# Optimization experiments

Measured on AMD Instinct MI355X. Metric: run time of the kernel, lower is better.

The kernel has to match this reference:

```python
import jax, jax.numpy as jnp
import numpy as np

B, T, E, H = 1, 2048, 2048, 32
D = E // H  # head_dim = 64


def alibi_bias(n_heads, t_q, t_k, dtype):
    # slopes: 2^(-8*(h+1)/n_heads) for power-of-two head counts
    slopes = jnp.power(2.0, -8.0 * jnp.arange(1, n_heads + 1, dtype=jnp.float32) / n_heads)
    i = jnp.arange(t_q)[:, None] + (t_k - t_q)  # absolute query positions
    j = jnp.arange(t_k)[None, :]
    rel = (j - i).astype(dtype)                 # [t_q, t_k], <=0 on/below diagonal
    return (slopes[:, None, None] * rel).astype(dtype)  # [H, t_q, t_k]


def setup_inputs() -> dict:
    key = jax.random.key(0)
    kx, kq, kk, kv, ko = jax.random.split(key, 5)
    s = E ** -0.5
    x = jax.random.normal(kx, (B, T, E), dtype=jnp.float32)
    Wq = jax.random.normal(kq, (E, E), dtype=jnp.float32) * s
    Wk = jax.random.normal(kk, (D, E), dtype=jnp.float32) * s
    Wv = jax.random.normal(kv, (D, E), dtype=jnp.float32) * s
    Wo = jax.random.normal(ko, (E, E), dtype=jnp.float32) * s
    # causal mask: True where attention is disallowed (j > i)
    attention_mask = jnp.triu(jnp.ones((T, T), dtype=bool), k=1)[None, None]  # [1,1,T,T]
    return {"x": x, "Wq": Wq, "Wk": Wk, "Wv": Wv, "Wo": Wo, "attention_mask": attention_mask}


def reference(x, Wq, Wk, Wv, Wo, attention_mask):
    b, t, _ = x.shape
    scale = D ** -0.5
    q = (x @ Wq.T).reshape(b, t, H, D).transpose(0, 2, 1, 3)  # [b,H,t,D]
    k = x @ Wk.T                                              # [b,t,D] (single KV head)
    v = x @ Wv.T                                              # [b,t,D]
    attn = jnp.einsum('bhtd,bsd->bhts', q * scale, k)         # [b,H,t,t]
    attn = attn + alibi_bias(H, t, t, attn.dtype)[None]
    attn = jnp.where(attention_mask, jnp.asarray(-10000.0, attn.dtype), attn)
    w = jax.nn.softmax(attn, axis=-1)
    out = jnp.einsum('bhts,bsd->bhtd', w, v)                  # [b,H,t,D]
    out = out.transpose(0, 2, 1, 3).reshape(b, t, E)
    return out @ Wo.T
```

## Files before the change

### kernel.cpp

```cpp
#include <hip/hip_runtime.h>
#include <stdint.h>

typedef __bf16 bf16;
typedef __bf16 bf16x4 __attribute__((ext_vector_type(4)));
typedef __bf16 bf16x8 __attribute__((ext_vector_type(8)));
typedef short short4v __attribute__((ext_vector_type(4)));
typedef float floatx4 __attribute__((ext_vector_type(4)));

#define MFMA32(a, b, c) __builtin_amdgcn_mfma_f32_16x16x32_bf16((a), (b), (c), 0, 0, 0)

__device__ __forceinline__ floatx4 mfma16(bf16x4 a, bf16x4 b, floatx4 c) {
  return __builtin_amdgcn_mfma_f32_16x16x16bf16_1k(
      __builtin_bit_cast(short4v, a), __builtin_bit_cast(short4v, b), c, 0, 0, 0);
}

__device__ __forceinline__ void gload16(const void* g, void* l) {
  __builtin_amdgcn_global_load_lds(
      (const __attribute__((address_space(1))) void*)g,
      (__attribute__((address_space(3))) void*)l, 16, 0, 0);
}

__device__ __forceinline__ bf16x8 load8(const float* p) {
  float4 lo = *(const float4*)p;
  float4 hi = *(const float4*)(p + 4);
  bf16x8 r;
  r[0] = (bf16)lo.x; r[1] = (bf16)lo.y; r[2] = (bf16)lo.z; r[3] = (bf16)lo.w;
  r[4] = (bf16)hi.x; r[5] = (bf16)hi.y; r[6] = (bf16)hi.z; r[7] = (bf16)hi.w;
  return r;
}

__global__ __launch_bounds__(256) void conv3(const float* __restrict__ a, bf16* __restrict__ ab,
                                             const float* __restrict__ b, bf16* __restrict__ bb,
                                             const float* __restrict__ c, bf16* __restrict__ cb) {
  const int i = blockIdx.x * 256 + threadIdx.x;
  const float* src = blockIdx.y == 0 ? a : (blockIdx.y == 1 ? b : c);
  bf16* dst = blockIdx.y == 0 ? ab : (blockIdx.y == 1 ? bb : cb);
  ((bf16x8*)dst)[i] = load8(src + (size_t)i * 8);
}

__global__ __launch_bounds__(256) void pack_kv(const float* __restrict__ Kf,
                                               const float* __restrict__ Vf,
                                               bf16* __restrict__ Kb,
                                               bf16* __restrict__ Vtb) {
  int i = blockIdx.x * 256 + threadIdx.x;
  if (i < 2048 * 64) {
    Kb[i] = (bf16)Kf[i];
    const int t = i >> 6, d = i & 63;
    Vtb[(size_t)d * 2048 + t] = (bf16)Vf[i];
  }
}

template <typename TC>
__global__ __launch_bounds__(256) void gemm_bt_a(const bf16* __restrict__ A,
                                                 const bf16* __restrict__ B,
                                                 TC* __restrict__ C,
                                                 int M, int N, int K) {
  __shared__ __align__(16) bf16 As[2][128 * 32];
  __shared__ __align__(16) bf16 Bs[2][128 * 32];
  const int tid = threadIdx.x;
  const int wave = tid >> 6, lane = tid & 63;
  const int quad = lane >> 4, l16 = lane & 15;
  const int m0 = blockIdx.y * 128, n0 = blockIdx.x * 128;
  const int wm = (wave >> 1) * 64, wn = (wave & 1) * 64;

  floatx4 acc[4][4];
#pragma unroll
  for (int i = 0; i < 4; i++)
#pragma unroll
    for (int j = 0; j < 4; j++) acc[i][j] = (floatx4)0.f;

  const int srow = tid >> 2, scol = (tid & 3) * 8;
  const bf16* Ap = A + (size_t)(m0 + srow) * K + scol;
  const bf16* Bp = B + (size_t)(n0 + srow) * K + scol;

  auto stage = [&](int k0, int buf) {
    char* a = (char*)As[buf] + tid * 16;
    char* b = (char*)Bs[buf] + tid * 16;
    gload16(Ap + k0, a);
    gload16(Ap + (size_t)64 * K + k0, a + 4096);
    gload16(Bp + k0, b);
    gload16(Bp + (size_t)64 * K + k0, b + 4096);
  };
  auto compute = [&](int buf) {
    bf16x8 af[4], bfr[4];
#pragma unroll
    for (int mt = 0; mt < 4; mt++)
      af[mt] = *(const bf16x8*)(&As[buf][(wm + mt * 16 + l16) * 32 + quad * 8]);
#pragma unroll
    for (int nt = 0; nt < 4; nt++)
      bfr[nt] = *(const bf16x8*)(&Bs[buf][(wn + nt * 16 + l16) * 32 + quad * 8]);
#pragma unroll
    for (int mt = 0; mt < 4; mt++)
#pragma unroll
      for (int nt = 0; nt < 4; nt++)
        acc[mt][nt] = MFMA32(af[mt], bfr[nt], acc[mt][nt]);
  };

  stage(0, 0);
  for (int k0 = 0; k0 < K; k0 += 64) {
    __syncthreads();
    if (k0 + 32 < K) stage(k0 + 32, 1);
    compute(0);
    __syncthreads();
    if (k0 + 64 < K) stage(k0 + 64, 0);
    compute(1);
  }

#pragma unroll
  for (int mt = 0; mt < 4; mt++) {
#pragma unroll
    for (int nt = 0; nt < 4; nt++) {
      const int col = n0 + wn + nt * 16 + l16;
      const int row = m0 + wm + mt * 16 + quad * 4;
#pragma unroll
      for (int r = 0; r < 4; r++)
        C[(size_t)(row + r) * N + col] = (TC)acc[mt][nt][r];
    }
  }
}

__global__ __launch_bounds__(256) void kv_gemm(const bf16* __restrict__ xb,
                                               const float* __restrict__ Wk,
                                               const float* __restrict__ Wv,
                                               float* __restrict__ Kf,
                                               float* __restrict__ Vf) {
  __shared__ __align__(16) bf16 As[128 * 40];
  __shared__ __align__(16) bf16 Bs[128 * 40];
  const int tid = threadIdx.x;
  const int wave = tid >> 6, lane = tid & 63;
  const int quad = lane >> 4, l16 = lane & 15;
  const int m0 = blockIdx.y * 128;
  const int kbeg = blockIdx.x * 256, kend = kbeg + 256;
  const int wm = (wave >> 1) * 64, wn = (wave & 1) * 64;

  floatx4 acc[4][4];
#pragma unroll
  for (int i = 0; i < 4; i++)
#pragma unroll
    for (int j = 0; j < 4; j++) acc[i][j] = (floatx4)0.f;

  const int sr = tid >> 2, sc = (tid & 3) * 8;

  for (int k0 = kbeg; k0 < kend; k0 += 32) {
    __syncthreads();
#pragma unroll
    for (int rr = 0; rr < 2; rr++) {
      const int row = sr + rr * 64;
      *(bf16x8*)(&As[row * 40 + sc]) =
          *(const bf16x8*)(&xb[(size_t)(m0 + row) * 2048 + k0 + sc]);
      const float* bsrc = (row < 64) ? &Wk[(size_t)row * 2048 + k0 + sc]
                                     : &Wv[(size_t)(row - 64) * 2048 + k0 + sc];
      *(bf16x8*)(&Bs[row * 40 + sc]) = load8(bsrc);
    }
    __syncthreads();

    bf16x8 af[4], bfr[4];
#pragma unroll
    for (int mt = 0; mt < 4; mt++)
      af[mt] = *(const bf16x8*)(&As[(wm + mt * 16 + l16) * 40 + quad * 8]);
#pragma unroll
    for (int nt = 0; nt < 4; nt++)
      bfr[nt] = *(const bf16x8*)(&Bs[(wn + nt * 16 + l16) * 40 + quad * 8]);
#pragma unroll
    for (int mt = 0; mt < 4; mt++)
#pragma unroll
      for (int nt = 0; nt < 4; nt++)
        acc[mt][nt] = MFMA32(af[mt], bfr[nt], acc[mt][nt]);
  }

#pragma unroll
  for (int mt = 0; mt < 4; mt++) {
#pragma unroll
    for (int nt = 0; nt < 4; nt++) {
      const int col = wn + nt * 16 + l16;
      const int row = m0 + wm + mt * 16 + quad * 4;
      float* dst = (col < 64) ? &Kf[(size_t)row * 64 + col]
                              : &Vf[(size_t)row * 64 + (col - 64)];
#pragma unroll
      for (int r = 0; r < 4; r++) atomicAdd(dst + (size_t)r * 64, acc[mt][nt][r]);
    }
  }
}

__global__ __launch_bounds__(256) void attn_kernel(const bf16* __restrict__ Q,
                                                   const bf16* __restrict__ Kb,
                                                   const bf16* __restrict__ Vtb,
                                                   bf16* __restrict__ O) {
  __shared__ __align__(16) bf16 Ks[64 * 72];
  __shared__ __align__(16) bf16 Vt[64 * 72];
  const int tid = threadIdx.x;
  const int wq = tid >> 6, lane = tid & 63;
  const int quad = lane >> 4, l16 = lane & 15;
  const int h = blockIdx.y;
  const float scale2 = 0.125f * 1.44269504f;
  const float slope2 = exp2f(-0.25f * (float)(h + 1)) * 1.44269504f;

  float cst[4][4];
#pragma unroll
  for (int mt = 0; mt < 4; mt++)
#pragma unroll
    for (int r = 0; r < 4; r++)
      cst[mt][r] = slope2 * (float)(mt * 16 + quad * 4 + r);

  const int r0 = tid >> 3, c0 = (tid & 7) * 8;

  auto run_tile = [&](int t) {
    const int qi = t * 64 + wq * 16 + l16;
    bf16x8 qf[2];
#pragma unroll
    for (int kk = 0; kk < 2; kk++)
      qf[kk] = *(const bf16x8*)(&Q[(size_t)qi * 2048 + h * 64 + kk * 32 + quad * 8]);

    floatx4 oacc[4];
#pragma unroll
    for (int dt = 0; dt < 4; dt++) oacc[dt] = (floatx4)0.f;
    float l_part = 0.f;

    bf16x8 kreg[2], vreg[2];
    kreg[0] = *(const bf16x8*)(&Kb[(size_t)r0 * 64 + c0]);
    kreg[1] = *(const bf16x8*)(&Kb[(size_t)(r0 + 32) * 64 + c0]);
    vreg[0] = *(const bf16x8*)(&Vtb[(size_t)r0 * 2048 + c0]);
    vreg[1] = *(const bf16x8*)(&Vtb[(size_t)(r0 + 32) * 2048 + c0]);

    for (int kt = 0; kt <= t; kt++) {
      __syncthreads();
      *(bf16x8*)(&Ks[r0 * 72 + c0]) = kreg[0];
      *(bf16x8*)(&Ks[(r0 + 32) * 72 + c0]) = kreg[1];
      *(bf16x8*)(&Vt[r0 * 72 + c0]) = vreg[0];
      *(bf16x8*)(&Vt[(r0 + 32) * 72 + c0]) = vreg[1];
      __syncthreads();
      if (kt < t) {
        const int kn = (kt + 1) * 64;
        kreg[0] = *(const bf16x8*)(&Kb[(size_t)(kn + r0) * 64 + c0]);
        kreg[1] = *(const bf16x8*)(&Kb[(size_t)(kn + r0 + 32) * 64 + c0]);
        vreg[0] = *(const bf16x8*)(&Vtb[(size_t)r0 * 2048 + kn + c0]);
        vreg[1] = *(const bf16x8*)(&Vtb[(size_t)(r0 + 32) * 2048 + kn + c0]);
      }
      const int k0 = kt * 64;

      floatx4 s[4];
#pragma unroll
      for (int mt = 0; mt < 4; mt++) s[mt] = (floatx4)0.f;
#pragma unroll
      for (int kk = 0; kk < 2; kk++) {
#pragma unroll
        for (int mt = 0; mt < 4; mt++) {
          bf16x8 kf = *(const bf16x8*)(&Ks[(mt * 16 + l16) * 72 + kk * 32 + quad * 8]);
          s[mt] = MFMA32(kf, qf[kk], s[mt]);
        }
      }

      const float base = slope2 * (float)(k0 - qi);
      bf16x4 pb[4];
      if (kt < t) {
#pragma unroll
        for (int mt = 0; mt < 4; mt++) {
          bf16x4 tb;
#pragma unroll
          for (int r = 0; r < 4; r++) {
            const float p = exp2f(__builtin_fmaf(s[mt][r], scale2, base + cst[mt][r]));
            l_part += p;
            tb[r] = (bf16)p;
          }
          pb[mt] = tb;
        }
      } else {
        const int qloc = qi - k0;
#pragma unroll
        for (int mt = 0; mt < 4; mt++) {
          bf16x4 tb;
#pragma unroll
          for (int r = 0; r < 4; r++) {
            const int moff = mt * 16 + quad * 4 + r;
            float p = exp2f(__builtin_fmaf(s[mt][r], scale2, base + cst[mt][r]));
            p = (moff <= qloc) ? p : 0.f;
            l_part += p;
            tb[r] = (bf16)p;
          }
          pb[mt] = tb;
        }
      }

#pragma unroll
      for (int dt = 0; dt < 4; dt++)
#pragma unroll
        for (int mt = 0; mt < 4; mt++) {
          const bf16x4 va = *(const bf16x4*)(&Vt[(dt * 16 + l16) * 72 + mt * 16 + quad * 4]);
          oacc[dt] = mfma16(va, pb[mt], oacc[dt]);
        }
    }

    float lf = l_part;
    lf += __shfl_xor(lf, 16);
    lf += __shfl_xor(lf, 32);
    const float linv = 1.0f / lf;
#pragma unroll
    for (int dt = 0; dt < 4; dt++) {
      bf16x4 ob;
#pragma unroll
      for (int r = 0; r < 4; r++) ob[r] = (bf16)(oacc[dt][r] * linv);
      *(bf16x4*)(&O[(size_t)qi * 2048 + h * 64 + dt * 16 + quad * 4]) = ob;
    }
  };

  run_tile(blockIdx.x);
  run_tile(31 - blockIdx.x);
}

extern "C" void kernel_launch(void* const* d_in, const int* in_sizes, int n_in,
                              void* d_out, int out_size, void* d_ws,
                              size_t ws_size, hipStream_t stream) {
  (void)in_sizes; (void)n_in; (void)out_size; (void)ws_size;
  const float* x = (const float*)d_in[0];
  const float* Wq = (const float*)d_in[1];
  const float* Wk = (const float*)d_in[2];
  const float* Wv = (const float*)d_in[3];
  const float* Wo = (const float*)d_in[4];
  float* out = (float*)d_out;

  const size_t NE = (size_t)2048 * 2048;
  bf16* xb = (bf16*)d_ws;
  bf16* Wqb = xb + NE;
  bf16* Wob = Wqb + NE;
  bf16* Qb = Wob + NE;
  float* Kf = (float*)(Qb + NE);
  float* Vf = Kf + 2048 * 64;
  bf16* Kb = (bf16*)(Vf + 2048 * 64);
  bf16* Vtb = Kb + 2048 * 64;
  bf16* AO = xb;

  hipMemsetAsync(Kf, 0, 2 * 2048 * 64 * sizeof(float), stream);
  conv3<<<dim3(2048, 3), 256, 0, stream>>>(x, xb, Wq, Wqb, Wo, Wob);
  gemm_bt_a<bf16><<<dim3(16, 16), 256, 0, stream>>>(xb, Wqb, Qb, 2048, 2048, 2048);
  kv_gemm<<<dim3(8, 16), 256, 0, stream>>>(xb, Wk, Wv, Kf, Vf);
  pack_kv<<<512, 256, 0, stream>>>(Kf, Vf, Kb, Vtb);
  attn_kernel<<<dim3(16, 32), 256, 0, stream>>>(Qb, Kb, Vtb, AO);
  gemm_bt_a<float><<<dim3(16, 16), 256, 0, stream>>>(AO, Wob, out, 2048, 2048, 2048);
}
```

Baseline: 262.4 us.

## Halve GEMM M-tile, launch one attention tile per block, row sums via MFMA

The GEMM tile shrinks from 128x128 to 64x128, doubling the grid to 512 blocks so the device's compute units have more blocks to fill. The attention kernel now processes one query tile per block across 1024 blocks, largest tiles first, instead of pairing tiles inside each block. Softmax row sums move from scalar adds and shuffles to an MFMA against a vector of ones, and the per-tile ALiBi constants are computed incrementally. The smaller GEMM tile lowers data reuse per block and adds a little MFMA work, and the row sum is now accumulated from bf16-rounded probabilities.

```diff
diff --git a/kernel.cpp b/kernel.cpp
--- a/kernel.cpp
+++ b/kernel.cpp
@@ -55,17 +55,17 @@
                                                  const bf16* __restrict__ B,
                                                  TC* __restrict__ C,
                                                  int M, int N, int K) {
-  __shared__ __align__(16) bf16 As[2][128 * 32];
+  __shared__ __align__(16) bf16 As[2][64 * 32];
   __shared__ __align__(16) bf16 Bs[2][128 * 32];
   const int tid = threadIdx.x;
   const int wave = tid >> 6, lane = tid & 63;
   const int quad = lane >> 4, l16 = lane & 15;
-  const int m0 = blockIdx.y * 128, n0 = blockIdx.x * 128;
-  const int wm = (wave >> 1) * 64, wn = (wave & 1) * 64;
-
-  floatx4 acc[4][4];
-#pragma unroll
-  for (int i = 0; i < 4; i++)
+  const int m0 = blockIdx.y * 64, n0 = blockIdx.x * 128;
+  const int wm = (wave >> 1) * 32, wn = (wave & 1) * 64;
+
+  floatx4 acc[2][4];
+#pragma unroll
+  for (int i = 0; i < 2; i++)
 #pragma unroll
     for (int j = 0; j < 4; j++) acc[i][j] = (floatx4)0.f;
 
@@ -74,23 +74,20 @@
   const bf16* Bp = B + (size_t)(n0 + srow) * K + scol;
 
   auto stage = [&](int k0, int buf) {
-    char* a = (char*)As[buf] + tid * 16;
-    char* b = (char*)Bs[buf] + tid * 16;
-    gload16(Ap + k0, a);
-    gload16(Ap + (size_t)64 * K + k0, a + 4096);
-    gload16(Bp + k0, b);
-    gload16(Bp + (size_t)64 * K + k0, b + 4096);
+    gload16(Ap + k0, (char*)As[buf] + tid * 16);
+    gload16(Bp + k0, (char*)Bs[buf] + tid * 16);
+    gload16(Bp + (size_t)64 * K + k0, (char*)Bs[buf] + 4096 + tid * 16);
   };
   auto compute = [&](int buf) {
-    bf16x8 af[4], bfr[4];
-#pragma unroll
-    for (int mt = 0; mt < 4; mt++)
+    bf16x8 af[2], bfr[4];
+#pragma unroll
+    for (int mt = 0; mt < 2; mt++)
       af[mt] = *(const bf16x8*)(&As[buf][(wm + mt * 16 + l16) * 32 + quad * 8]);
 #pragma unroll
     for (int nt = 0; nt < 4; nt++)
       bfr[nt] = *(const bf16x8*)(&Bs[buf][(wn + nt * 16 + l16) * 32 + quad * 8]);
 #pragma unroll
-    for (int mt = 0; mt < 4; mt++)
+    for (int mt = 0; mt < 2; mt++)
 #pragma unroll
       for (int nt = 0; nt < 4; nt++)
         acc[mt][nt] = MFMA32(af[mt], bfr[nt], acc[mt][nt]);
@@ -107,7 +104,7 @@
   }
 
 #pragma unroll
-  for (int mt = 0; mt < 4; mt++) {
+  for (int mt = 0; mt < 2; mt++) {
 #pragma unroll
     for (int nt = 0; nt < 4; nt++) {
       const int col = n0 + wn + nt * 16 + l16;
@@ -192,119 +189,112 @@
   const int wq = tid >> 6, lane = tid & 63;
   const int quad = lane >> 4, l16 = lane & 15;
   const int h = blockIdx.y;
+  const int t = 31 - blockIdx.x;
   const float scale2 = 0.125f * 1.44269504f;
   const float slope2 = exp2f(-0.25f * (float)(h + 1)) * 1.44269504f;
 
-  float cst[4][4];
-#pragma unroll
-  for (int mt = 0; mt < 4; mt++)
-#pragma unroll
-    for (int r = 0; r < 4; r++)
-      cst[mt][r] = slope2 * (float)(mt * 16 + quad * 4 + r);
+  float cq[4];
+#pragma unroll
+  for (int r = 0; r < 4; r++) cq[r] = slope2 * (float)(quad * 4 + r);
+  const float s16 = slope2 * 16.f;
 
   const int r0 = tid >> 3, c0 = (tid & 7) * 8;
 
-  auto run_tile = [&](int t) {
-    const int qi = t * 64 + wq * 16 + l16;
-    bf16x8 qf[2];
-#pragma unroll
-    for (int kk = 0; kk < 2; kk++)
-      qf[kk] = *(const bf16x8*)(&Q[(size_t)qi * 2048 + h * 64 + kk * 32 + quad * 8]);
-
-    floatx4 oacc[4];
-#pragma unroll
-    for (int dt = 0; dt < 4; dt++) oacc[dt] = (floatx4)0.f;
-    float l_part = 0.f;
-
-    bf16x8 kreg[2], vreg[2];
-    kreg[0] = *(const bf16x8*)(&Kb[(size_t)r0 * 64 + c0]);
-    kreg[1] = *(const bf16x8*)(&Kb[(size_t)(r0 + 32) * 64 + c0]);
-    vreg[0] = *(const bf16x8*)(&Vtb[(size_t)r0 * 2048 + c0]);
-    vreg[1] = *(const bf16x8*)(&Vtb[(size_t)(r0 + 32) * 2048 + c0]);
-
-    for (int kt = 0; kt <= t; kt++) {
-      __syncthreads();
-      *(bf16x8*)(&Ks[r0 * 72 + c0]) = kreg[0];
-      *(bf16x8*)(&Ks[(r0 + 32) * 72 + c0]) = kreg[1];
-      *(bf16x8*)(&Vt[r0 * 72 + c0]) = vreg[0];
-      *(bf16x8*)(&Vt[(r0 + 32) * 72 + c0]) = vreg[1];
-      __syncthreads();
-      if (kt < t) {
-        const int kn = (kt + 1) * 64;
-        kreg[0] = *(const bf16x8*)(&Kb[(size_t)(kn + r0) * 64 + c0]);
-        kreg[1] = *(const bf16x8*)(&Kb[(size_t)(kn + r0 + 32) * 64 + c0]);
-        vreg[0] = *(const bf16x8*)(&Vtb[(size_t)r0 * 2048 + kn + c0]);
-        vreg[1] = *(const bf16x8*)(&Vtb[(size_t)(r0 + 32) * 2048 + kn + c0]);
+  const int qi = t * 64 + wq * 16 + l16;
+  bf16x8 qf[2];
+#pragma unroll
+  for (int kk = 0; kk < 2; kk++)
+    qf[kk] = *(const bf16x8*)(&Q[(size_t)qi * 2048 + h * 64 + kk * 32 + quad * 8]);
+
+  floatx4 oacc[4];
+#pragma unroll
+  for (int dt = 0; dt < 4; dt++) oacc[dt] = (floatx4)0.f;
+  floatx4 lacc = (floatx4)0.f;
+  const bf16x4 ones = {(bf16)1.f, (bf16)1.f, (bf16)1.f, (bf16)1.f};
+
+  bf16x8 kreg[2], vreg[2];
+  kreg[0] = *(const bf16x8*)(&Kb[(size_t)r0 * 64 + c0]);
+  kreg[1] = *(const bf16x8*)(&Kb[(size_t)(r0 + 32) * 64 + c0]);
+  vreg[0] = *(const bf16x8*)(&Vtb[(size_t)r0 * 2048 + c0]);
+  vreg[1] = *(const bf16x8*)(&Vtb[(size_t)(r0 + 32) * 2048 + c0]);
+
+  for (int kt = 0; kt <= t; kt++) {
+    __syncthreads();
+    *(bf16x8*)(&Ks[r0 * 72 + c0]) = kreg[0];
+    *(bf16x8*)(&Ks[(r0 + 32) * 72 + c0]) = kreg[1];
+    *(bf16x8*)(&Vt[r0 * 72 + c0]) = vreg[0];
+    *(bf16x8*)(&Vt[(r0 + 32) * 72 + c0]) = vreg[1];
+    __syncthreads();
+    if (kt < t) {
+      const int kn = (kt + 1) * 64;
+      kreg[0] = *(const bf16x8*)(&Kb[(size_t)(kn + r0) * 64 + c0]);
+      kreg[1] = *(const bf16x8*)(&Kb[(size_t)(kn + r0 + 32) * 64 + c0]);
+      vreg[0] = *(const bf16x8*)(&Vtb[(size_t)r0 * 2048 + kn + c0]);
+      vreg[1] = *(const bf16x8*)(&Vtb[(size_t)(r0 + 32) * 2048 + kn + c0]);
+    }
+    const int k0 = kt * 64;
+
+    floatx4 s[4];
+#pragma unroll
+    for (int mt = 0; mt < 4; mt++) s[mt] = (floatx4)0.f;
+#pragma unroll
+    for (int kk = 0; kk < 2; kk++) {
+#pragma unroll
+      for (int mt = 0; mt < 4; mt++) {
+        bf16x8 kf = *(const bf16x8*)(&Ks[(mt * 16 + l16) * 72 + kk * 32 + quad * 8]);
+        s[mt] = MFMA32(kf, qf[kk], s[mt]);
       }
-      const int k0 = kt * 64;
-
-      floatx4 s[4];
-#pragma unroll
-      for (int mt = 0; mt < 4; mt++) s[mt] = (floatx4)0.f;
-#pragma unroll
-      for (int kk = 0; kk < 2; kk++) {
-#pragma unroll
-        for (int mt = 0; mt < 4; mt++) {
-          bf16x8 kf = *(const bf16x8*)(&Ks[(mt * 16 + l16) * 72 + kk * 32 + quad * 8]);
-          s[mt] = MFMA32(kf, qf[kk], s[mt]);
+    }
+
+    const float base0 = slope2 * (float)(k0 - qi);
+    bf16x4 pb[4];
+    if (kt < t) {
+      float base = base0;
+#pragma unroll
+      for (int mt = 0; mt < 4; mt++) {
+        bf16x4 tb;
+#pragma unroll
+        for (int r = 0; r < 4; r++)
+          tb[r] = (bf16)exp2f(__builtin_fmaf(s[mt][r], scale2, base + cq[r]));
+        pb[mt] = tb;
+        base += s16;
+      }
+    } else {
+      const int qloc = qi - k0;
+      float base = base0;
+#pragma unroll
+      for (int mt = 0; mt < 4; mt++) {
+        bf16x4 tb;
+#pragma unroll
+        for (int r = 0; r < 4; r++) {
+          const int moff = mt * 16 + quad * 4 + r;
+          const float p = exp2f(__builtin_fmaf(s[mt][r], scale2, base + cq[r]));
+          tb[r] = (moff <= qloc) ? (bf16)p : (bf16)0.f;
         }
+        pb[mt] = tb;
+        base += s16;
       }
-
-      const float base = slope2 * (float)(k0 - qi);
-      bf16x4 pb[4];
-      if (kt < t) {
-#pragma unroll
-        for (int mt = 0; mt < 4; mt++) {
-          bf16x4 tb;
-#pragma unroll
-          for (int r = 0; r < 4; r++) {
-            const float p = exp2f(__builtin_fmaf(s[mt][r], scale2, base + cst[mt][r]));
-            l_part += p;
-            tb[r] = (bf16)p;
-          }
-          pb[mt] = tb;
-        }
-      } else {
-        const int qloc = qi - k0;
-#pragma unroll
-        for (int mt = 0; mt < 4; mt++) {
-          bf16x4 tb;
-#pragma unroll
-          for (int r = 0; r < 4; r++) {
-            const int moff = mt * 16 + quad * 4 + r;
-            float p = exp2f(__builtin_fmaf(s[mt][r], scale2, base + cst[mt][r]));
-            p = (moff <= qloc) ? p : 0.f;
-            l_part += p;
-            tb[r] = (bf16)p;
-          }
-          pb[mt] = tb;
-        }
+    }
+
+#pragma unroll
+    for (int mt = 0; mt < 4; mt++) {
+      lacc = mfma16(ones, pb[mt], lacc);
+#pragma unroll
+      for (int dt = 0; dt < 4; dt++) {
+        const bf16x4 va = *(const bf16x4*)(&Vt[(dt * 16 + l16) * 72 + mt * 16 + quad * 4]);
+        oacc[dt] = mfma16(va, pb[mt], oacc[dt]);
       }
-
-#pragma unroll
-      for (int dt = 0; dt < 4; dt++)
-#pragma unroll
-        for (int mt = 0; mt < 4; mt++) {
-          const bf16x4 va = *(const bf16x4*)(&Vt[(dt * 16 + l16) * 72 + mt * 16 + quad * 4]);
-          oacc[dt] = mfma16(va, pb[mt], oacc[dt]);
-        }
-    }
-
-    float lf = l_part;
-    lf += __shfl_xor(lf, 16);
-    lf += __shfl_xor(lf, 32);
-    const float linv = 1.0f / lf;
-#pragma unroll
-    for (int dt = 0; dt < 4; dt++) {
-      bf16x4 ob;
-#pragma unroll
-      for (int r = 0; r < 4; r++) ob[r] = (bf16)(oacc[dt][r] * linv);
-      *(bf16x4*)(&O[(size_t)qi * 2048 + h * 64 + dt * 16 + quad * 4]) = ob;
-    }
-  };
-
-  run_tile(blockIdx.x);
-  run_tile(31 - blockIdx.x);
+    }
+  }
+
+  const float linv = 1.0f / lacc[0];
+#pragma unroll
+  for (int dt = 0; dt < 4; dt++) {
+    bf16x4 ob;
+#pragma unroll
+    for (int r = 0; r < 4; r++) ob[r] = (bf16)(oacc[dt][r] * linv);
+    *(bf16x4*)(&O[(size_t)qi * 2048 + h * 64 + dt * 16 + quad * 4]) = ob;
+  }
 }
 
 extern "C" void kernel_launch(void* const* d_in, const int* in_sizes, int n_in,
@@ -331,9 +321,9 @@
 
   hipMemsetAsync(Kf, 0, 2 * 2048 * 64 * sizeof(float), stream);
   conv3<<<dim3(2048, 3), 256, 0, stream>>>(x, xb, Wq, Wqb, Wo, Wob);
-  gemm_bt_a<bf16><<<dim3(16, 16), 256, 0, stream>>>(xb, Wqb, Qb, 2048, 2048, 2048);
+  gemm_bt_a<bf16><<<dim3(16, 32), 256, 0, stream>>>(xb, Wqb, Qb, 2048, 2048, 2048);
   kv_gemm<<<dim3(8, 16), 256, 0, stream>>>(xb, Wk, Wv, Kf, Vf);
   pack_kv<<<512, 256, 0, stream>>>(Kf, Vf, Kb, Vtb);
-  attn_kernel<<<dim3(16, 32), 256, 0, stream>>>(Qb, Kb, Vtb, AO);
-  gemm_bt_a<float><<<dim3(16, 16), 256, 0, stream>>>(AO, Wob, out, 2048, 2048, 2048);
-}
+  attn_kernel<<<dim3(32, 32), 256, 0, stream>>>(Qb, Kb, Vtb, AO);
+  gemm_bt_a<float><<<dim3(16, 32), 256, 0, stream>>>(AO, Wob, out, 2048, 2048, 2048);
+}
```

Measured after the change: 276.5 us. 1.05x slower.
